# Performance work log

Hardware: AMD Instinct MI355X
Metric: run time of the kernel (lower is better)

Reference implementation:

```python
import jax, jax.numpy as jnp
import numpy as np

N_NODES = 50000
N_EDGES = 1600000
IN_DIM = 128
OUT_DIM = 64
HEADS = 4


def setup_inputs() -> dict:
    key = jax.random.key(0)
    k1, k2, k3, k4 = jax.random.split(key, 4)
    x = jax.random.normal(k1, (N_NODES, IN_DIM), dtype=jnp.float32)
    edge_index = jax.random.randint(k2, (2, N_EDGES), 0, N_NODES, dtype=jnp.int64)
    # W[h]: per-head linear weight (in_dim -> out_dim), no bias
    W = jax.random.normal(k3, (HEADS, IN_DIM, OUT_DIM), dtype=jnp.float32) * 0.1
    # a[h]: attention vector over concat([h_src, h_dst]) -> scalar, no bias
    a = jax.random.normal(k4, (HEADS, 2 * OUT_DIM), dtype=jnp.float32) * 0.1
    return {"x": x, "edge_index": edge_index, "W": W, "a": a}


def reference(x, edge_index, W, a):
    n_nodes = x.shape[0]
    out_dim = W.shape[2]
    src, dst = edge_index[0], edge_index[1]
    # per-head projection: [N, H, O]
    h = jnp.einsum('nf,hfo->nho', x, W)
    h_src = h[src]  # [E, H, O]
    h_dst = h[dst]  # [E, H, O]
    a_src, a_dst = a[:, :out_dim], a[:, out_dim:]  # split of concat weight
    # e = leaky_relu(a^T [h_src || h_dst]) per edge, per head: [E, H]
    e = jnp.einsum('eho,ho->eh', h_src, a_src) + jnp.einsum('eho,ho->eh', h_dst, a_dst)
    e = jax.nn.leaky_relu(e, negative_slope=0.01)
    # NOTE: faithful to source — softmax over ALL edges (dim=0), not per-dst
    alpha = jax.nn.softmax(e, axis=0)  # [E, H]
    msgs = h_src * alpha[:, :, None]  # [E, H, O]
    agg = jax.ops.segment_sum(msgs, dst, num_segments=n_nodes)  # [N, H, O]
    # concat heads along feature dim (head-major), matching torch.cat(out, dim=1)
    return agg.reshape(n_nodes, -1)
```

## Files before the change

### kernel.cpp

```cpp
#include <hip/hip_runtime.h>
#include <stdint.h>

#define N_NODES 50000
#define N_EDGES 1600000
#define IN_DIM  128
#define OUT_DIM 64
#define HEADS   4
#define HO      (HEADS*OUT_DIM)

typedef __attribute__((ext_vector_type(8))) short short8;
typedef __attribute__((ext_vector_type(8))) unsigned short bf16x8;
typedef __attribute__((ext_vector_type(4))) float f32x4;

__device__ __forceinline__ unsigned fenc(float f) {
    unsigned u = __float_as_uint(f);
    return (u & 0x80000000u) ? ~u : (u | 0x80000000u);
}
__device__ __forceinline__ float fdec(unsigned u) {
    return __uint_as_float((u & 0x80000000u) ? (u ^ 0x80000000u) : ~u);
}
__device__ __forceinline__ float lrelu(float v) {
    return v >= 0.f ? v : 0.01f * v;
}
__device__ __forceinline__ unsigned short f2bf(float f) {
    unsigned u = __float_as_uint(f);
    return (unsigned short)((u + 0x7FFFu + ((u >> 16) & 1u)) >> 16);
}
__device__ __forceinline__ float bf2f(unsigned short b) {
    return __uint_as_float(((unsigned)b) << 16);
}

#define HIST_BLOCKS  1024
#define XCONV_BLOCKS 1024
#define WT_BLOCKS    32

__global__ __launch_bounds__(256) void k_prep_hist(
    const float* __restrict__ x, const float* __restrict__ W,
    const int* __restrict__ edst,
    unsigned short* __restrict__ xb, unsigned short* __restrict__ wt,
    int* __restrict__ cnt, int* __restrict__ rank)
{
    int b = blockIdx.x;
    if (b < HIST_BLOCKS) {
        const int stride = HIST_BLOCKS * 256;
        for (int e = b * 256 + threadIdx.x; e < N_EDGES; e += stride)
            rank[e] = atomicAdd(&cnt[edst[e]], 1);
        return;
    }
    b -= HIST_BLOCKS;
    if (b < XCONV_BLOCKS) {
        const int total4 = N_NODES * IN_DIM / 4;
        const int stride = XCONV_BLOCKS * 256;
        for (int i = b * 256 + threadIdx.x; i < total4; i += stride) {
            float4 v = ((const float4*)x)[i];
            ushort4 u;
            u.x = f2bf(v.x); u.y = f2bf(v.y); u.z = f2bf(v.z); u.w = f2bf(v.w);
            ((ushort4*)xb)[i] = u;
        }
        return;
    }
    b -= XCONV_BLOCKS;
    {
        int item = b * 256 + threadIdx.x;
        int n  = item >> 5;
        int k0 = (item & 31) * 4;
        int h = n >> 6, o = n & 63;
        const float* wp = &W[((size_t)h * IN_DIM + k0) * OUT_DIM + o];
        ushort4 u;
        u.x = f2bf(wp[0 * OUT_DIM]);
        u.y = f2bf(wp[1 * OUT_DIM]);
        u.z = f2bf(wp[2 * OUT_DIM]);
        u.w = f2bf(wp[3 * OUT_DIM]);
        *(ushort4*)&wt[(size_t)n * IN_DIM + k0] = u;
    }
}

#define BM 64
#define GEMM_BLOCKS ((N_NODES + BM - 1) / BM)

__global__ __launch_bounds__(256) void k_gemm(
    const unsigned short* __restrict__ xb, const unsigned short* __restrict__ wt,
    const float* __restrict__ a,
    unsigned short* __restrict__ hb, float* __restrict__ s_src, float* __restrict__ s_dst)
{
    extern __shared__ char smem[];
    char* Alds = smem;
    char* Blds = smem + 16384;

    const int tid  = threadIdx.x;
    const int wave = tid >> 6;
    const int lane = tid & 63;
    const int node0 = blockIdx.x * BM;

    {
        const char* xsrc = (const char*)xb + (size_t)node0 * 256;
        #pragma unroll
        for (int j = 0; j < 4; ++j) {
            int o = (j * 256 + tid) * 16;
            uint4 v = *(const uint4*)(xsrc + o);
            int sw = o ^ (((o >> 8) & 7) << 4);
            *(uint4*)(Alds + sw) = v;
        }
    }
    {
        const char* wsrc = (const char*)wt;
        #pragma unroll
        for (int j = 0; j < 16; ++j) {
            int o = (j * 256 + tid) * 16;
            uint4 v = *(const uint4*)(wsrc + o);
            int sw = o ^ (((o >> 8) & 7) << 4);
            *(uint4*)(Blds + sw) = v;
        }
    }
    __syncthreads();

    const int wr0  = wave * 16;
    const int l15  = lane & 15;
    const int lhi  = lane >> 4;
    const int kxor = (lane & 7) << 4;

    short8 af[4];
    #pragma unroll
    for (int s = 0; s < 4; ++s)
        af[s] = *(const short8*)(Alds + (wr0 + l15) * 256 + ((s * 64 + lhi * 16) ^ kxor));

    f32x4 acc[16];
    #pragma unroll
    for (int nt = 0; nt < 16; ++nt) acc[nt] = (f32x4){0.f, 0.f, 0.f, 0.f};

    #pragma unroll
    for (int nt = 0; nt < 16; ++nt) {
        const char* bbase = Blds + (nt * 16 + l15) * 256;
        #pragma unroll
        for (int s = 0; s < 4; ++s) {
            short8 bf = *(const short8*)(bbase + ((s * 64 + lhi * 16) ^ kxor));
            acc[nt] = __builtin_amdgcn_mfma_f32_16x16x32_bf16(af[s], bf, acc[nt], 0, 0, 0);
        }
    }

    #pragma unroll
    for (int nt = 0; nt < 16; ++nt) {
        int col = nt * 16 + l15;
        #pragma unroll
        for (int r = 0; r < 4; ++r) {
            int node = node0 + wr0 + lhi * 4 + r;
            if (node < N_NODES)
                hb[(size_t)node * HO + col] = f2bf(acc[nt][r]);
        }
    }

    #pragma unroll
    for (int h = 0; h < 4; ++h) {
        float avs0 = a[h*128 +  0 + l15], avs1 = a[h*128 + 16 + l15];
        float avs2 = a[h*128 + 32 + l15], avs3 = a[h*128 + 48 + l15];
        float avd0 = a[h*128 + 64 + l15], avd1 = a[h*128 + 80 + l15];
        float avd2 = a[h*128 + 96 + l15], avd3 = a[h*128 + 112 + l15];
        #pragma unroll
        for (int r = 0; r < 4; ++r) {
            float vs = acc[4*h+0][r]*avs0 + acc[4*h+1][r]*avs1
                     + acc[4*h+2][r]*avs2 + acc[4*h+3][r]*avs3;
            float vd = acc[4*h+0][r]*avd0 + acc[4*h+1][r]*avd1
                     + acc[4*h+2][r]*avd2 + acc[4*h+3][r]*avd3;
            #pragma unroll
            for (int m = 8; m >= 1; m >>= 1) {
                vs += __shfl_xor(vs, m);
                vd += __shfl_xor(vd, m);
            }
            int node = node0 + wr0 + lhi * 4 + r;
            if (l15 == 0 && node < N_NODES) {
                s_src[node * HEADS + h] = vs;
                s_dst[node * HEADS + h] = vd;
            }
        }
    }
}

__global__ __launch_bounds__(1024) void k_scan(
    const int* __restrict__ cnt, int* __restrict__ row_start)
{
    __shared__ int part[1024];
    const int t  = threadIdx.x;
    const int CH = (N_NODES + 1023) / 1024;
    const int lo = t * CH;
    const int hi = (lo + CH < N_NODES) ? lo + CH : N_NODES;

    int s = 0;
    for (int i = lo; i < hi; ++i) s += cnt[i];
    part[t] = s;
    __syncthreads();

    for (int off = 1; off < 1024; off <<= 1) {
        int v = (t >= off) ? part[t - off] : 0;
        __syncthreads();
        part[t] += v;
        __syncthreads();
    }

    int run = (t == 0) ? 0 : part[t - 1];
    for (int i = lo; i < hi; ++i) {
        row_start[i] = run;
        run += cnt[i];
    }
    if (t == 1023) row_start[N_NODES] = part[1023];
}

__global__ __launch_bounds__(256) void k_nodemax(
    const float* __restrict__ s_src, const float* __restrict__ s_dst,
    unsigned* __restrict__ gmax_src, unsigned* __restrict__ gmax_dst)
{
    float4 ms = make_float4(-1e30f, -1e30f, -1e30f, -1e30f);
    float4 md = ms;
    const int stride = gridDim.x * blockDim.x;
    for (int n = blockIdx.x * blockDim.x + threadIdx.x; n < N_NODES; n += stride) {
        float4 vs = ((const float4*)s_src)[n];
        float4 vd = ((const float4*)s_dst)[n];
        ms.x = fmaxf(ms.x, vs.x); ms.y = fmaxf(ms.y, vs.y);
        ms.z = fmaxf(ms.z, vs.z); ms.w = fmaxf(ms.w, vs.w);
        md.x = fmaxf(md.x, vd.x); md.y = fmaxf(md.y, vd.y);
        md.z = fmaxf(md.z, vd.z); md.w = fmaxf(md.w, vd.w);
    }
    #pragma unroll
    for (int m = 32; m >= 1; m >>= 1) {
        ms.x = fmaxf(ms.x, __shfl_xor(ms.x, m)); ms.y = fmaxf(ms.y, __shfl_xor(ms.y, m));
        ms.z = fmaxf(ms.z, __shfl_xor(ms.z, m)); ms.w = fmaxf(ms.w, __shfl_xor(ms.w, m));
        md.x = fmaxf(md.x, __shfl_xor(md.x, m)); md.y = fmaxf(md.y, __shfl_xor(md.y, m));
        md.z = fmaxf(md.z, __shfl_xor(md.z, m)); md.w = fmaxf(md.w, __shfl_xor(md.w, m));
    }
    if ((threadIdx.x & 63) == 0) {
        atomicMax(&gmax_src[0], fenc(ms.x)); atomicMax(&gmax_src[1], fenc(ms.y));
        atomicMax(&gmax_src[2], fenc(ms.z)); atomicMax(&gmax_src[3], fenc(ms.w));
        atomicMax(&gmax_dst[0], fenc(md.x)); atomicMax(&gmax_dst[1], fenc(md.y));
        atomicMax(&gmax_dst[2], fenc(md.z)); atomicMax(&gmax_dst[3], fenc(md.w));
    }
}

#define BUCKET_BLOCKS 512
__global__ __launch_bounds__(256) void k_bucket(
    const int* __restrict__ esrc, const int* __restrict__ edst,
    const int* __restrict__ rank, const int* __restrict__ row_start,
    const float* __restrict__ s_src, const float* __restrict__ s_dst,
    const unsigned* __restrict__ gmax_src, const unsigned* __restrict__ gmax_dst,
    int* __restrict__ sorted_src, double* __restrict__ gsum)
{
    const float mx0 = lrelu(fdec(gmax_src[0]) + fdec(gmax_dst[0]));
    const float mx1 = lrelu(fdec(gmax_src[1]) + fdec(gmax_dst[1]));
    const float mx2 = lrelu(fdec(gmax_src[2]) + fdec(gmax_dst[2]));
    const float mx3 = lrelu(fdec(gmax_src[3]) + fdec(gmax_dst[3]));
    double a0 = 0.0, a1 = 0.0, a2 = 0.0, a3 = 0.0;
    const int stride = gridDim.x * blockDim.x;
    for (int e = blockIdx.x * blockDim.x + threadIdx.x; e < N_EDGES; e += stride) {
        int s = esrc[e], d = edst[e];
        sorted_src[row_start[d] + rank[e]] = s;
        float4 ss = *(const float4*)&s_src[s * HEADS];
        float4 sd = *(const float4*)&s_dst[d * HEADS];
        a0 += (double)__expf(lrelu(ss.x + sd.x) - mx0);
        a1 += (double)__expf(lrelu(ss.y + sd.y) - mx1);
        a2 += (double)__expf(lrelu(ss.z + sd.z) - mx2);
        a3 += (double)__expf(lrelu(ss.w + sd.w) - mx3);
    }
    #pragma unroll
    for (int m = 32; m >= 1; m >>= 1) {
        a0 += __shfl_xor(a0, m); a1 += __shfl_xor(a1, m);
        a2 += __shfl_xor(a2, m); a3 += __shfl_xor(a3, m);
    }
    __shared__ double part[4][4];
    const int wave = threadIdx.x >> 6;
    if ((threadIdx.x & 63) == 0) {
        part[wave][0] = a0; part[wave][1] = a1; part[wave][2] = a2; part[wave][3] = a3;
    }
    __syncthreads();
    if (threadIdx.x < 4) {
        double t = part[0][threadIdx.x] + part[1][threadIdx.x]
                 + part[2][threadIdx.x] + part[3][threadIdx.x];
        atomicAdd(&gsum[threadIdx.x], t);
    }
}

__global__ __launch_bounds__(256) void k_agg(
    const int* __restrict__ row_start, const int* __restrict__ sorted_src,
    const unsigned short* __restrict__ hb,
    const float* __restrict__ s_src, const float* __restrict__ s_dst,
    const unsigned* __restrict__ gmax_src, const unsigned* __restrict__ gmax_dst,
    const double* __restrict__ gsum, float* __restrict__ out)
{
    const int wid = (int)((blockIdx.x * 256u + threadIdx.x) >> 6);
    if (wid >= N_NODES) return;
    const int lane = threadIdx.x & 63;
    const int half = lane >> 5;
    const int l32  = lane & 31;
    const int head = l32 >> 3;
    const int og   = (l32 & 7) * 8;
    const int hoff = head * OUT_DIM + og;

    const int beg = row_start[wid];
    const int end = row_start[wid + 1];
    const float mx  = lrelu(fdec(gmax_src[head]) + fdec(gmax_dst[head]));
    const float inv = (float)(1.0 / gsum[head]);
    const float sd  = s_dst[wid * HEADS + head];

    float c0=0.f,c1=0.f,c2=0.f,c3=0.f,c4=0.f,c5=0.f,c6=0.f,c7=0.f;

    int j = beg + half;
    for (; j + 2 < end; j += 4) {
        int sA = sorted_src[j];
        int sB = sorted_src[j + 2];
        float pA = __expf(lrelu(s_src[sA * HEADS + head] + sd) - mx) * inv;
        float pB = __expf(lrelu(s_src[sB * HEADS + head] + sd) - mx) * inv;
        bf16x8 uA = *(const bf16x8*)&hb[(size_t)sA * HO + hoff];
        bf16x8 uB = *(const bf16x8*)&hb[(size_t)sB * HO + hoff];
        c0 = fmaf(pA, bf2f(uA[0]), c0); c1 = fmaf(pA, bf2f(uA[1]), c1);
        c2 = fmaf(pA, bf2f(uA[2]), c2); c3 = fmaf(pA, bf2f(uA[3]), c3);
        c4 = fmaf(pA, bf2f(uA[4]), c4); c5 = fmaf(pA, bf2f(uA[5]), c5);
        c6 = fmaf(pA, bf2f(uA[6]), c6); c7 = fmaf(pA, bf2f(uA[7]), c7);
        c0 = fmaf(pB, bf2f(uB[0]), c0); c1 = fmaf(pB, bf2f(uB[1]), c1);
        c2 = fmaf(pB, bf2f(uB[2]), c2); c3 = fmaf(pB, bf2f(uB[3]), c3);
        c4 = fmaf(pB, bf2f(uB[4]), c4); c5 = fmaf(pB, bf2f(uB[5]), c5);
        c6 = fmaf(pB, bf2f(uB[6]), c6); c7 = fmaf(pB, bf2f(uB[7]), c7);
    }
    for (; j < end; j += 2) {
        int sA = sorted_src[j];
        float pA = __expf(lrelu(s_src[sA * HEADS + head] + sd) - mx) * inv;
        bf16x8 uA = *(const bf16x8*)&hb[(size_t)sA * HO + hoff];
        c0 = fmaf(pA, bf2f(uA[0]), c0); c1 = fmaf(pA, bf2f(uA[1]), c1);
        c2 = fmaf(pA, bf2f(uA[2]), c2); c3 = fmaf(pA, bf2f(uA[3]), c3);
        c4 = fmaf(pA, bf2f(uA[4]), c4); c5 = fmaf(pA, bf2f(uA[5]), c5);
        c6 = fmaf(pA, bf2f(uA[6]), c6); c7 = fmaf(pA, bf2f(uA[7]), c7);
    }

    c0 += __shfl_xor(c0, 32); c1 += __shfl_xor(c1, 32);
    c2 += __shfl_xor(c2, 32); c3 += __shfl_xor(c3, 32);
    c4 += __shfl_xor(c4, 32); c5 += __shfl_xor(c5, 32);
    c6 += __shfl_xor(c6, 32); c7 += __shfl_xor(c7, 32);

    float4 v = half ? make_float4(c4, c5, c6, c7) : make_float4(c0, c1, c2, c3);
    *(float4*)&out[(size_t)wid * HO + hoff + half * 4] = v;
}

extern "C" void kernel_launch(void* const* d_in, const int* in_sizes, int n_in,
                              void* d_out, int out_size, void* d_ws, size_t ws_size,
                              hipStream_t stream)
{
    const float* x    = (const float*)d_in[0];
    const int*   eidx = (const int*)d_in[1];
    const float* W    = (const float*)d_in[2];
    const float* a    = (const float*)d_in[3];
    float* out = (float*)d_out;

    unsigned short* hb = (unsigned short*)d_ws;
    unsigned short* xb = hb + (size_t)N_NODES * HO;
    unsigned short* wt = xb + (size_t)N_NODES * IN_DIM;
    float*    s_src    = (float*)(wt + (size_t)HO * IN_DIM);
    float*    s_dst    = s_src + (size_t)N_NODES * HEADS;
    double*   gsum     = (double*)(s_dst + (size_t)N_NODES * HEADS);
    unsigned* gmax_src = (unsigned*)(gsum + 4);
    unsigned* gmax_dst = gmax_src + 4;
    int*      cnt      = (int*)(gmax_dst + 4);
    int*      row_start = cnt + N_NODES;
    int*      rank     = row_start + (N_NODES + 1);
    int*      sorted_src = rank + N_EDGES;

    const int* esrc = eidx;
    const int* edst = eidx + N_EDGES;

    hipMemsetAsync(gsum, 0, 4 * sizeof(double) + 8 * sizeof(unsigned) + N_NODES * sizeof(int),
                   stream);

    k_prep_hist<<<HIST_BLOCKS + XCONV_BLOCKS + WT_BLOCKS, 256, 0, stream>>>(
        x, W, edst, xb, wt, cnt, rank);
    k_gemm<<<GEMM_BLOCKS, 256, 81920, stream>>>(xb, wt, a, hb, s_src, s_dst);
    k_scan<<<1, 1024, 0, stream>>>(cnt, row_start);
    k_nodemax<<<64, 256, 0, stream>>>(s_src, s_dst, gmax_src, gmax_dst);
    k_bucket<<<BUCKET_BLOCKS, 256, 0, stream>>>(
        esrc, edst, rank, row_start, s_src, s_dst, gmax_src, gmax_dst, sorted_src, gsum);
    k_agg<<<(N_NODES * 64 + 255) / 256, 256, 0, stream>>>(
        row_start, sorted_src, hb, s_src, s_dst, gmax_src, gmax_dst, gsum, out);
}
```

Measured before the change: 360.1 us.

## Fold scan and node-max into GEMM, precompute bf16 edge weights in bucket pass

The standalone scan and node-max kernels are removed. An extra GEMM block now does the prefix scan, and each GEMM wave reduces the per-head max of its attention scores and updates the global max atomically. The bucket pass now writes a 12-byte record per sorted edge holding the source index and four bf16 exp weights, and accumulates the softmax denominator from those rounded values. The aggregation kernel then skips the gathers of s_src and s_dst and the exp work, and unrolls 4 edges per iteration. In exchange it reads larger per-edge records, adds bf16 rounding to the attention weights, and the scan block must wait for the histogram to finish while the GEMM runs.

```diff
diff --git a/kernel.cpp b/kernel.cpp
--- a/kernel.cpp
+++ b/kernel.cpp
@@ -81,9 +81,37 @@
 __global__ __launch_bounds__(256) void k_gemm(
     const unsigned short* __restrict__ xb, const unsigned short* __restrict__ wt,
     const float* __restrict__ a,
-    unsigned short* __restrict__ hb, float* __restrict__ s_src, float* __restrict__ s_dst)
+    const int* __restrict__ cnt, int* __restrict__ row_start,
+    unsigned short* __restrict__ hb, float* __restrict__ s_src, float* __restrict__ s_dst,
+    unsigned* __restrict__ gmax_src, unsigned* __restrict__ gmax_dst)
 {
     extern __shared__ char smem[];
+
+    if (blockIdx.x == GEMM_BLOCKS) {
+        int* part = (int*)smem;
+        const int t  = threadIdx.x;
+        const int CH = (N_NODES + 255) / 256;
+        const int lo = t * CH;
+        const int hi = (lo + CH < N_NODES) ? lo + CH : N_NODES;
+        int s = 0;
+        for (int i = lo; i < hi; ++i) s += cnt[i];
+        part[t] = s;
+        __syncthreads();
+        for (int off = 1; off < 256; off <<= 1) {
+            int v = (t >= off) ? part[t - off] : 0;
+            __syncthreads();
+            part[t] += v;
+            __syncthreads();
+        }
+        int run = (t == 0) ? 0 : part[t - 1];
+        for (int i = lo; i < hi; ++i) {
+            row_start[i] = run;
+            run += cnt[i];
+        }
+        if (t == 255) row_start[N_NODES] = part[255];
+        return;
+    }
+
     char* Alds = smem;
     char* Blds = smem + 16384;
 
@@ -155,6 +183,7 @@
         float avs2 = a[h*128 + 32 + l15], avs3 = a[h*128 + 48 + l15];
         float avd0 = a[h*128 + 64 + l15], avd1 = a[h*128 + 80 + l15];
         float avd2 = a[h*128 + 96 + l15], avd3 = a[h*128 + 112 + l15];
+        float mS = -1e30f, mD = -1e30f;
         #pragma unroll
         for (int r = 0; r < 4; ++r) {
             float vs = acc[4*h+0][r]*avs0 + acc[4*h+1][r]*avs1
@@ -167,70 +196,20 @@
                 vd += __shfl_xor(vd, m);
             }
             int node = node0 + wr0 + lhi * 4 + r;
-            if (l15 == 0 && node < N_NODES) {
+            bool ok = node < N_NODES;
+            if (l15 == 0 && ok) {
                 s_src[node * HEADS + h] = vs;
                 s_dst[node * HEADS + h] = vd;
             }
-        }
-    }
-}
-
-__global__ __launch_bounds__(1024) void k_scan(
-    const int* __restrict__ cnt, int* __restrict__ row_start)
-{
-    __shared__ int part[1024];
-    const int t  = threadIdx.x;
-    const int CH = (N_NODES + 1023) / 1024;
-    const int lo = t * CH;
-    const int hi = (lo + CH < N_NODES) ? lo + CH : N_NODES;
-
-    int s = 0;
-    for (int i = lo; i < hi; ++i) s += cnt[i];
-    part[t] = s;
-    __syncthreads();
-
-    for (int off = 1; off < 1024; off <<= 1) {
-        int v = (t >= off) ? part[t - off] : 0;
-        __syncthreads();
-        part[t] += v;
-        __syncthreads();
-    }
-
-    int run = (t == 0) ? 0 : part[t - 1];
-    for (int i = lo; i < hi; ++i) {
-        row_start[i] = run;
-        run += cnt[i];
-    }
-    if (t == 1023) row_start[N_NODES] = part[1023];
-}
-
-__global__ __launch_bounds__(256) void k_nodemax(
-    const float* __restrict__ s_src, const float* __restrict__ s_dst,
-    unsigned* __restrict__ gmax_src, unsigned* __restrict__ gmax_dst)
-{
-    float4 ms = make_float4(-1e30f, -1e30f, -1e30f, -1e30f);
-    float4 md = ms;
-    const int stride = gridDim.x * blockDim.x;
-    for (int n = blockIdx.x * blockDim.x + threadIdx.x; n < N_NODES; n += stride) {
-        float4 vs = ((const float4*)s_src)[n];
-        float4 vd = ((const float4*)s_dst)[n];
-        ms.x = fmaxf(ms.x, vs.x); ms.y = fmaxf(ms.y, vs.y);
-        ms.z = fmaxf(ms.z, vs.z); ms.w = fmaxf(ms.w, vs.w);
-        md.x = fmaxf(md.x, vd.x); md.y = fmaxf(md.y, vd.y);
-        md.z = fmaxf(md.z, vd.z); md.w = fmaxf(md.w, vd.w);
-    }
-    #pragma unroll
-    for (int m = 32; m >= 1; m >>= 1) {
-        ms.x = fmaxf(ms.x, __shfl_xor(ms.x, m)); ms.y = fmaxf(ms.y, __shfl_xor(ms.y, m));
-        ms.z = fmaxf(ms.z, __shfl_xor(ms.z, m)); ms.w = fmaxf(ms.w, __shfl_xor(ms.w, m));
-        md.x = fmaxf(md.x, __shfl_xor(md.x, m)); md.y = fmaxf(md.y, __shfl_xor(md.y, m));
-        md.z = fmaxf(md.z, __shfl_xor(md.z, m)); md.w = fmaxf(md.w, __shfl_xor(md.w, m));
-    }
-    if ((threadIdx.x & 63) == 0) {
-        atomicMax(&gmax_src[0], fenc(ms.x)); atomicMax(&gmax_src[1], fenc(ms.y));
-        atomicMax(&gmax_src[2], fenc(ms.z)); atomicMax(&gmax_src[3], fenc(ms.w));
-        atomicMax(&gmax_dst[0], fenc(md.x)); atomicMax(&gmax_dst[1], fenc(md.y));
-        atomicMax(&gmax_dst[2], fenc(md.z)); atomicMax(&gmax_dst[3], fenc(md.w));
+            mS = fmaxf(mS, ok ? vs : -1e30f);
+            mD = fmaxf(mD, ok ? vd : -1e30f);
+        }
+        mS = fmaxf(mS, __shfl_xor(mS, 16)); mS = fmaxf(mS, __shfl_xor(mS, 32));
+        mD = fmaxf(mD, __shfl_xor(mD, 16)); mD = fmaxf(mD, __shfl_xor(mD, 32));
+        if (lane == 0) {
+            atomicMax(&gmax_src[h], fenc(mS));
+            atomicMax(&gmax_dst[h], fenc(mD));
+        }
     }
 }
 
@@ -240,7 +219,7 @@
     const int* __restrict__ rank, const int* __restrict__ row_start,
     const float* __restrict__ s_src, const float* __restrict__ s_dst,
     const unsigned* __restrict__ gmax_src, const unsigned* __restrict__ gmax_dst,
-    int* __restrict__ sorted_src, double* __restrict__ gsum)
+    unsigned* __restrict__ rec, double* __restrict__ gsum)
 {
     const float mx0 = lrelu(fdec(gmax_src[0]) + fdec(gmax_dst[0]));
     const float mx1 = lrelu(fdec(gmax_src[1]) + fdec(gmax_dst[1]));
@@ -250,13 +229,20 @@
     const int stride = gridDim.x * blockDim.x;
     for (int e = blockIdx.x * blockDim.x + threadIdx.x; e < N_EDGES; e += stride) {
         int s = esrc[e], d = edst[e];
-        sorted_src[row_start[d] + rank[e]] = s;
+        int pos = row_start[d] + rank[e];
         float4 ss = *(const float4*)&s_src[s * HEADS];
         float4 sd = *(const float4*)&s_dst[d * HEADS];
-        a0 += (double)__expf(lrelu(ss.x + sd.x) - mx0);
-        a1 += (double)__expf(lrelu(ss.y + sd.y) - mx1);
-        a2 += (double)__expf(lrelu(ss.z + sd.z) - mx2);
-        a3 += (double)__expf(lrelu(ss.w + sd.w) - mx3);
+        unsigned b0 = f2bf(__expf(lrelu(ss.x + sd.x) - mx0));
+        unsigned b1 = f2bf(__expf(lrelu(ss.y + sd.y) - mx1));
+        unsigned b2 = f2bf(__expf(lrelu(ss.z + sd.z) - mx2));
+        unsigned b3 = f2bf(__expf(lrelu(ss.w + sd.w) - mx3));
+        rec[(size_t)pos * 3 + 0] = (unsigned)s;
+        rec[(size_t)pos * 3 + 1] = b0 | (b1 << 16);
+        rec[(size_t)pos * 3 + 2] = b2 | (b3 << 16);
+        a0 += (double)bf2f((unsigned short)b0);
+        a1 += (double)bf2f((unsigned short)b1);
+        a2 += (double)bf2f((unsigned short)b2);
+        a3 += (double)bf2f((unsigned short)b3);
     }
     #pragma unroll
     for (int m = 32; m >= 1; m >>= 1) {
@@ -277,10 +263,8 @@
 }
 
 __global__ __launch_bounds__(256) void k_agg(
-    const int* __restrict__ row_start, const int* __restrict__ sorted_src,
+    const int* __restrict__ row_start, const unsigned* __restrict__ rec,
     const unsigned short* __restrict__ hb,
-    const float* __restrict__ s_src, const float* __restrict__ s_dst,
-    const unsigned* __restrict__ gmax_src, const unsigned* __restrict__ gmax_dst,
     const double* __restrict__ gsum, float* __restrict__ out)
 {
     const int wid = (int)((blockIdx.x * 256u + threadIdx.x) >> 6);
@@ -294,45 +278,43 @@
 
     const int beg = row_start[wid];
     const int end = row_start[wid + 1];
-    const float mx  = lrelu(fdec(gmax_src[head]) + fdec(gmax_dst[head]));
     const float inv = (float)(1.0 / gsum[head]);
-    const float sd  = s_dst[wid * HEADS + head];
 
     float c0=0.f,c1=0.f,c2=0.f,c3=0.f,c4=0.f,c5=0.f,c6=0.f,c7=0.f;
 
+    #define EDGE(rc)                                                            \
+        {                                                                       \
+            unsigned aw = (head & 2) ? (rc).z : (rc).y;                         \
+            float p = bf2f((unsigned short)((head & 1) ? (aw >> 16)             \
+                                                       : (aw & 0xFFFFu)));      \
+            bf16x8 u = *(const bf16x8*)&hb[(size_t)(rc).x * HO + hoff];         \
+            c0 = fmaf(p, bf2f(u[0]), c0); c1 = fmaf(p, bf2f(u[1]), c1);         \
+            c2 = fmaf(p, bf2f(u[2]), c2); c3 = fmaf(p, bf2f(u[3]), c3);         \
+            c4 = fmaf(p, bf2f(u[4]), c4); c5 = fmaf(p, bf2f(u[5]), c5);         \
+            c6 = fmaf(p, bf2f(u[6]), c6); c7 = fmaf(p, bf2f(u[7]), c7);         \
+        }
+
     int j = beg + half;
-    for (; j + 2 < end; j += 4) {
-        int sA = sorted_src[j];
-        int sB = sorted_src[j + 2];
-        float pA = __expf(lrelu(s_src[sA * HEADS + head] + sd) - mx) * inv;
-        float pB = __expf(lrelu(s_src[sB * HEADS + head] + sd) - mx) * inv;
-        bf16x8 uA = *(const bf16x8*)&hb[(size_t)sA * HO + hoff];
-        bf16x8 uB = *(const bf16x8*)&hb[(size_t)sB * HO + hoff];
-        c0 = fmaf(pA, bf2f(uA[0]), c0); c1 = fmaf(pA, bf2f(uA[1]), c1);
-        c2 = fmaf(pA, bf2f(uA[2]), c2); c3 = fmaf(pA, bf2f(uA[3]), c3);
-        c4 = fmaf(pA, bf2f(uA[4]), c4); c5 = fmaf(pA, bf2f(uA[5]), c5);
-        c6 = fmaf(pA, bf2f(uA[6]), c6); c7 = fmaf(pA, bf2f(uA[7]), c7);
-        c0 = fmaf(pB, bf2f(uB[0]), c0); c1 = fmaf(pB, bf2f(uB[1]), c1);
-        c2 = fmaf(pB, bf2f(uB[2]), c2); c3 = fmaf(pB, bf2f(uB[3]), c3);
-        c4 = fmaf(pB, bf2f(uB[4]), c4); c5 = fmaf(pB, bf2f(uB[5]), c5);
-        c6 = fmaf(pB, bf2f(uB[6]), c6); c7 = fmaf(pB, bf2f(uB[7]), c7);
+    for (; j + 6 < end; j += 8) {
+        uint3 rA = *(const uint3*)&rec[(size_t)j * 3];
+        uint3 rB = *(const uint3*)&rec[(size_t)(j + 2) * 3];
+        uint3 rC = *(const uint3*)&rec[(size_t)(j + 4) * 3];
+        uint3 rD = *(const uint3*)&rec[(size_t)(j + 6) * 3];
+        EDGE(rA); EDGE(rB); EDGE(rC); EDGE(rD);
     }
     for (; j < end; j += 2) {
-        int sA = sorted_src[j];
-        float pA = __expf(lrelu(s_src[sA * HEADS + head] + sd) - mx) * inv;
-        bf16x8 uA = *(const bf16x8*)&hb[(size_t)sA * HO + hoff];
-        c0 = fmaf(pA, bf2f(uA[0]), c0); c1 = fmaf(pA, bf2f(uA[1]), c1);
-        c2 = fmaf(pA, bf2f(uA[2]), c2); c3 = fmaf(pA, bf2f(uA[3]), c3);
-        c4 = fmaf(pA, bf2f(uA[4]), c4); c5 = fmaf(pA, bf2f(uA[5]), c5);
-        c6 = fmaf(pA, bf2f(uA[6]), c6); c7 = fmaf(pA, bf2f(uA[7]), c7);
-    }
+        uint3 rA = *(const uint3*)&rec[(size_t)j * 3];
+        EDGE(rA);
+    }
+    #undef EDGE
 
     c0 += __shfl_xor(c0, 32); c1 += __shfl_xor(c1, 32);
     c2 += __shfl_xor(c2, 32); c3 += __shfl_xor(c3, 32);
     c4 += __shfl_xor(c4, 32); c5 += __shfl_xor(c5, 32);
     c6 += __shfl_xor(c6, 32); c7 += __shfl_xor(c7, 32);
 
-    float4 v = half ? make_float4(c4, c5, c6, c7) : make_float4(c0, c1, c2, c3);
+    float4 v = half ? make_float4(c4 * inv, c5 * inv, c6 * inv, c7 * inv)
+                    : make_float4(c0 * inv, c1 * inv, c2 * inv, c3 * inv);
     *(float4*)&out[(size_t)wid * HO + hoff + half * 4] = v;
 }
 
@@ -356,8 +338,8 @@
     unsigned* gmax_dst = gmax_src + 4;
     int*      cnt      = (int*)(gmax_dst + 4);
     int*      row_start = cnt + N_NODES;
-    int*      rank     = row_start + (N_NODES + 1);
-    int*      sorted_src = rank + N_EDGES;
+    int*      rank     = row_start + (N_NODES + 2);
+    unsigned* rec      = (unsigned*)(rank + N_EDGES);
 
     const int* esrc = eidx;
     const int* edst = eidx + N_EDGES;
@@ -367,11 +349,10 @@
 
     k_prep_hist<<<HIST_BLOCKS + XCONV_BLOCKS + WT_BLOCKS, 256, 0, stream>>>(
         x, W, edst, xb, wt, cnt, rank);
-    k_gemm<<<GEMM_BLOCKS, 256, 81920, stream>>>(xb, wt, a, hb, s_src, s_dst);
-    k_scan<<<1, 1024, 0, stream>>>(cnt, row_start);
-    k_nodemax<<<64, 256, 0, stream>>>(s_src, s_dst, gmax_src, gmax_dst);
+    k_gemm<<<GEMM_BLOCKS + 1, 256, 81920, stream>>>(
+        xb, wt, a, cnt, row_start, hb, s_src, s_dst, gmax_src, gmax_dst);
     k_bucket<<<BUCKET_BLOCKS, 256, 0, stream>>>(
-        esrc, edst, rank, row_start, s_src, s_dst, gmax_src, gmax_dst, sorted_src, gsum);
+        esrc, edst, rank, row_start, s_src, s_dst, gmax_src, gmax_dst, rec, gsum);
     k_agg<<<(N_NODES * 64 + 255) / 256, 256, 0, stream>>>(
-        row_start, sorted_src, hb, s_src, s_dst, gmax_src, gmax_dst, gsum, out);
-}
+        row_start, rec, hb, gsum, out);
+}
```

Result: slower. 556.3 us, median of 2 (+54.5%).
